# Performance work log

Measured on AMD Instinct MI355X. Metric: run time of the kernel, lower is better.

Reference implementation:

```python
import jax, jax.numpy as jnp
import numpy as np

N, C, K = 400000, 32, 27
EPS = 1e-5


def sparse_conv(feats, W, nbr, mask):
    # feats [N,Cin], W [K,Cin,Cout], nbr [N,K] int, mask [N,K] bool
    g = feats[nbr] * mask[..., None]          # gather: [N,K,Cin]
    return jnp.einsum('nki,kio->no', g, W)    # per-offset GEMM + scatter-accumulate


def batchnorm(x, gamma, beta):
    # MinkowskiBatchNorm over all active points (axis 0), training-mode stats
    mean = jnp.mean(x, axis=0)
    var = jnp.var(x, axis=0)
    return (x - mean) * jax.lax.rsqrt(var + EPS) * gamma + beta


def setup_inputs() -> dict:
    key = jax.random.key(0)
    ks = jax.random.split(key, 8)
    feats = jax.random.normal(ks[0], (N, C), dtype=jnp.float32)
    nbr = jax.random.randint(ks[1], (N, K), 0, N, dtype=jnp.int32)
    mask = jax.random.randint(ks[2], (N, K), 0, 2, dtype=jnp.int32).astype(bool)
    scale = 1.0 / np.sqrt(K * C)
    W1 = jax.random.normal(ks[3], (K, C, C), dtype=jnp.float32) * scale
    W2 = jax.random.normal(ks[4], (K, C, C), dtype=jnp.float32) * scale
    gamma1 = jnp.ones((C,), jnp.float32)
    beta1 = jnp.zeros((C,), jnp.float32)
    gamma2 = jnp.ones((C,), jnp.float32)
    beta2 = jnp.zeros((C,), jnp.float32)
    return {"feats": feats, "W1": W1, "gamma1": gamma1, "beta1": beta1,
            "W2": W2, "gamma2": gamma2, "beta2": beta2,
            "nbr": nbr, "mask": mask}


def reference(feats, W1, gamma1, beta1, W2, gamma2, beta2, nbr, mask):
    h = sparse_conv(feats, W1, nbr, mask)
    h = jax.nn.relu(batchnorm(h, gamma1, beta1))
    h = sparse_conv(h, W2, nbr, mask)
    h = batchnorm(h, gamma2, beta2)
    # in_ch == out_ch -> identity residual (no downsample branch)
    return jax.nn.relu(h + feats)
```

## Files before the change

### kernel.cpp

```cpp
#include <hip/hip_runtime.h>

#define NPTS 400000
#define KOFF 27

typedef __attribute__((ext_vector_type(8))) __bf16 bf16x8;
typedef __attribute__((ext_vector_type(16))) float v16f;

__device__ __forceinline__ float bf2f(unsigned short u) {
  union { unsigned int i; float f; } v; v.i = ((unsigned int)u) << 16; return v.f;
}
__device__ __forceinline__ unsigned short f2bf(float f) {
  union { float f; unsigned int i; } v; v.f = f;
  unsigned int x = v.i;
  return (unsigned short)((x + 0x7FFFu + ((x >> 16) & 1u)) >> 16);
}

__global__ void prep_feats(const float* __restrict__ feats, unsigned short* __restrict__ Xb,
                           unsigned short* __restrict__ H1, float* __restrict__ statszero) {
  int idx = blockIdx.x * 256 + threadIdx.x;
  const float4* f4 = (const float4*)feats;
  float4 a = f4[2 * idx], b = f4[2 * idx + 1];
  union { unsigned short u[8]; uint4 v; } p;
  p.u[0] = f2bf(a.x); p.u[1] = f2bf(a.y); p.u[2] = f2bf(a.z); p.u[3] = f2bf(a.w);
  p.u[4] = f2bf(b.x); p.u[5] = f2bf(b.y); p.u[6] = f2bf(b.z); p.u[7] = f2bf(b.w);
  ((uint4*)Xb)[idx] = p.v;
  if (blockIdx.x == 0) {
    if (threadIdx.x < 32) {
      Xb[(size_t)NPTS * 32 + threadIdx.x] = 0;
      H1[(size_t)NPTS * 32 + threadIdx.x] = 0;
    }
    if (threadIdx.x < 128) statszero[threadIdx.x] = 0.f;
  }
}

__global__ void prep_nbr(const int* __restrict__ nbr, const int* __restrict__ mask,
                         int* __restrict__ nbrT) {
  int n = blockIdx.x * 256 + threadIdx.x;
  if (n >= NPTS) return;
  #pragma unroll
  for (int k = 0; k < KOFF; ++k) {
    int j = nbr[(size_t)n * KOFF + k];
    int m = mask[(size_t)n * KOFF + k];
    nbrT[(size_t)k * NPTS + n] = (m != 0) ? j : NPTS;
  }
}

__global__ void prep_w(const float* __restrict__ W1, const float* __restrict__ W2,
                       unsigned short* __restrict__ WT1, unsigned short* __restrict__ WT2) {
  int i = blockIdx.x * 256 + threadIdx.x;
  if (i >= 27 * 1024) return;
  int k = i >> 10, r = i & 1023, o = r >> 5, ic = r & 31;
  int src = k * 1024 + ic * 32 + o;
  WT1[i] = f2bf(W1[src]);
  WT2[i] = f2bf(W2[src]);
}

__global__ __launch_bounds__(256, 4) void conv_mfma(
    const unsigned short* __restrict__ X,
    const int* __restrict__ nbrT,
    const unsigned short* __restrict__ WT,
    unsigned short* __restrict__ Hout,
    float* __restrict__ stats)
{
  const int lane = threadIdx.x & 63;
  const int wv   = threadIdx.x >> 6;
  const int col  = lane & 31;
  const int hf   = lane >> 5;
  const int n0   = (blockIdx.x * 4 + wv) * 32;

  v16f acc;
  #pragma unroll
  for (int i = 0; i < 16; ++i) acc[i] = 0.0f;

  const int* nb = nbrT + n0 + col;
  const bf16x8* wp = (const bf16x8*)(WT + col * 32 + hf * 8);

  #pragma unroll 4
  for (int k = 0; k < KOFF; ++k) {
    int row = nb[k * NPTS];
    const bf16x8* ap = (const bf16x8*)(X + (size_t)row * 32 + hf * 8);
    bf16x8 a0 = ap[0];
    bf16x8 a1 = ap[2];
    bf16x8 b0 = wp[k * 128];
    bf16x8 b1 = wp[k * 128 + 2];
    acc = __builtin_amdgcn_mfma_f32_32x32x16_bf16(a0, b0, acc, 0, 0, 0);
    acc = __builtin_amdgcn_mfma_f32_32x32x16_bf16(a1, b1, acc, 0, 0, 0);
  }

  float s = 0.f, q = 0.f;
  #pragma unroll
  for (int r = 0; r < 16; ++r) {
    float v = acc[r];
    s += v; q += v * v;
    int rw = (r & 3) + 8 * (r >> 2) + 4 * hf;
    Hout[(size_t)(n0 + rw) * 32 + col] = f2bf(v);
  }
  s += __shfl_xor(s, 32);
  q += __shfl_xor(q, 32);
  __shared__ float redS[4][32];
  __shared__ float redQ[4][32];
  if (lane < 32) { redS[wv][col] = s; redQ[wv][col] = q; }
  __syncthreads();
  if (threadIdx.x < 64) {
    int t = threadIdx.x & 31;
    float v = (threadIdx.x < 32)
      ? (redS[0][t] + redS[1][t] + redS[2][t] + redS[3][t])
      : (redQ[0][t] + redQ[1][t] + redQ[2][t] + redQ[3][t]);
    atomicAdd(&stats[threadIdx.x], v);
  }
}

__global__ void finalize_bn(const float* __restrict__ stats, const float* __restrict__ gamma,
                            const float* __restrict__ beta, float* __restrict__ sb) {
  int t = threadIdx.x;
  if (t < 32) {
    float mean = stats[t] * (1.f / NPTS);
    float var  = stats[t + 32] * (1.f / NPTS) - mean * mean;
    float rstd = rsqrtf(var + 1e-5f);
    float sc = gamma[t] * rstd;
    sb[t] = sc;
    sb[t + 32] = beta[t] - mean * sc;
  }
}

__global__ void bn_relu_inplace(unsigned short* __restrict__ H, const float* __restrict__ sb) {
  int idx = blockIdx.x * 256 + threadIdx.x;
  uint4 v = ((uint4*)H)[idx];
  union { uint4 v; unsigned short u[8]; } p; p.v = v;
  int baseo = (idx * 8) & 31;
  #pragma unroll
  for (int j = 0; j < 8; ++j) {
    float f = bf2f(p.u[j]);
    f = fmaxf(f * sb[baseo + j] + sb[32 + baseo + j], 0.f);
    p.u[j] = f2bf(f);
  }
  ((uint4*)H)[idx] = p.v;
}

__global__ void bn_res_relu_out(const unsigned short* __restrict__ H2, const float* __restrict__ feats,
                                const float* __restrict__ sb, float* __restrict__ out) {
  int idx = blockIdx.x * 256 + threadIdx.x;
  uint4 v = ((const uint4*)H2)[idx];
  union { uint4 v; unsigned short u[8]; } p; p.v = v;
  int baseo = (idx * 8) & 31;
  const float4* f4 = (const float4*)feats;
  float4 fa = f4[2 * idx], fb = f4[2 * idx + 1];
  float4 o0, o1;
  float* fav = (float*)&fa; float* fbv = (float*)&fb;
  float* o0v = (float*)&o0; float* o1v = (float*)&o1;
  #pragma unroll
  for (int j = 0; j < 4; ++j)
    o0v[j] = fmaxf(bf2f(p.u[j]) * sb[baseo + j] + sb[32 + baseo + j] + fav[j], 0.f);
  #pragma unroll
  for (int j = 0; j < 4; ++j)
    o1v[j] = fmaxf(bf2f(p.u[4 + j]) * sb[baseo + 4 + j] + sb[32 + baseo + 4 + j] + fbv[j], 0.f);
  ((float4*)out)[2 * idx] = o0;
  ((float4*)out)[2 * idx + 1] = o1;
}

extern "C" void kernel_launch(void* const* d_in, const int* in_sizes, int n_in,
                              void* d_out, int out_size, void* d_ws, size_t ws_size,
                              hipStream_t stream) {
  const float* feats  = (const float*)d_in[0];
  const float* W1     = (const float*)d_in[1];
  const float* gamma1 = (const float*)d_in[2];
  const float* beta1  = (const float*)d_in[3];
  const float* W2     = (const float*)d_in[4];
  const float* gamma2 = (const float*)d_in[5];
  const float* beta2  = (const float*)d_in[6];
  const int*   nbr    = (const int*)d_in[7];
  const int*   mask   = (const int*)d_in[8];

  char* ws = (char*)d_ws;
  const size_t XB = ((size_t)(NPTS + 1) * 32 * 2 + 255) & ~(size_t)255;
  unsigned short* Xb   = (unsigned short*)(ws);
  unsigned short* H1   = (unsigned short*)(ws + XB);
  int*            nbrT = (int*)(ws + 2 * XB);
  size_t off = 2 * XB + (size_t)KOFF * NPTS * 4;
  unsigned short* WT1 = (unsigned short*)(ws + off); off += 27 * 1024 * 2;
  unsigned short* WT2 = (unsigned short*)(ws + off); off += 27 * 1024 * 2;
  float* stats1 = (float*)(ws + off); off += 256;
  float* stats2 = (float*)(ws + off); off += 256;
  float* sb1    = (float*)(ws + off); off += 256;
  float* sb2    = (float*)(ws + off); off += 256;
  unsigned short* H2 = Xb;

  prep_feats<<<6250, 256, 0, stream>>>(feats, Xb, H1, stats1);
  prep_nbr<<<1563, 256, 0, stream>>>(nbr, mask, nbrT);
  prep_w<<<108, 256, 0, stream>>>(W1, W2, WT1, WT2);

  conv_mfma<<<3125, 256, 0, stream>>>(Xb, nbrT, WT1, H1, stats1);
  finalize_bn<<<1, 64, 0, stream>>>(stats1, gamma1, beta1, sb1);
  bn_relu_inplace<<<6250, 256, 0, stream>>>(H1, sb1);

  conv_mfma<<<3125, 256, 0, stream>>>(H1, nbrT, WT2, H2, stats2);
  finalize_bn<<<1, 64, 0, stream>>>(stats2, gamma2, beta2, sb2);
  bn_res_relu_out<<<6250, 256, 0, stream>>>(H2, feats, sb2, (float*)d_out);
}
```

Baseline: 448.7 us.

## Switch conv to 16x16x32 MFMA with LDS-staged weights and fuse BN finalize

The conv kernel moves from 32x32x16 MFMA tiles to 16x16x32 tiles in 1024-thread blocks. All 27 offset weight fragments are preloaded into LDS in a lane-ready layout, and the next neighbor index is prefetched on each iteration. The neighbor-table transpose now goes through shared memory so global reads and writes are coalesced. The separate finalize_bn launches are folded into the BN/ReLU kernels, which each recompute scale and shift per block. This cuts global weight loads and launch count, at the cost of a 54KB LDS load per block and a heavy register and occupancy demand from the 1024-thread blocks.

```diff
diff --git a/kernel.cpp b/kernel.cpp
--- a/kernel.cpp
+++ b/kernel.cpp
@@ -4,7 +4,7 @@
 #define KOFF 27
 
 typedef __attribute__((ext_vector_type(8))) __bf16 bf16x8;
-typedef __attribute__((ext_vector_type(16))) float v16f;
+typedef __attribute__((ext_vector_type(4))) float v4f;
 
 __device__ __forceinline__ float bf2f(unsigned short u) {
   union { unsigned int i; float f; } v; v.i = ((unsigned int)u) << 16; return v.f;
@@ -35,95 +35,122 @@
 
 __global__ void prep_nbr(const int* __restrict__ nbr, const int* __restrict__ mask,
                          int* __restrict__ nbrT) {
-  int n = blockIdx.x * 256 + threadIdx.x;
-  if (n >= NPTS) return;
-  #pragma unroll
-  for (int k = 0; k < KOFF; ++k) {
-    int j = nbr[(size_t)n * KOFF + k];
-    int m = mask[(size_t)n * KOFF + k];
-    nbrT[(size_t)k * NPTS + n] = (m != 0) ? j : NPTS;
+  __shared__ int tile[256 * KOFF];
+  int p0 = blockIdx.x * 256;
+  int cnt = (NPTS - p0 < 256) ? (NPTS - p0) : 256;
+  int total = cnt * KOFF;
+  for (int i = threadIdx.x; i < total; i += 256) {
+    int j = nbr[(size_t)p0 * KOFF + i];
+    int mk = mask[(size_t)p0 * KOFF + i];
+    tile[i] = (mk != 0) ? j : NPTS;
+  }
+  __syncthreads();
+  int t = threadIdx.x;
+  if (t < cnt) {
+    #pragma unroll
+    for (int k = 0; k < KOFF; ++k)
+      nbrT[(size_t)k * NPTS + p0 + t] = tile[t * KOFF + k];
   }
 }
 
 __global__ void prep_w(const float* __restrict__ W1, const float* __restrict__ W2,
-                       unsigned short* __restrict__ WT1, unsigned short* __restrict__ WT2) {
-  int i = blockIdx.x * 256 + threadIdx.x;
-  if (i >= 27 * 1024) return;
-  int k = i >> 10, r = i & 1023, o = r >> 5, ic = r & 31;
-  int src = k * 1024 + ic * 32 + o;
-  WT1[i] = f2bf(W1[src]);
-  WT2[i] = f2bf(W2[src]);
-}
-
-__global__ __launch_bounds__(256, 4) void conv_mfma(
+                       unsigned short* __restrict__ WL1, unsigned short* __restrict__ WL2) {
+  int idx = blockIdx.x * 256 + threadIdx.x;
+  if (idx >= KOFF * 1024) return;
+  int k = idx >> 10, r = idx & 1023;
+  int h = r >> 9, rr = r & 511;
+  int lane = rr >> 3, j = rr & 7;
+  int i_ch = (lane >> 4) * 8 + j;
+  int o_ch = h * 16 + (lane & 15);
+  int src = k * 1024 + i_ch * 32 + o_ch;
+  WL1[idx] = f2bf(W1[src]);
+  WL2[idx] = f2bf(W2[src]);
+}
+
+__global__ __launch_bounds__(1024, 8) void conv_mfma16(
     const unsigned short* __restrict__ X,
     const int* __restrict__ nbrT,
-    const unsigned short* __restrict__ WT,
+    const unsigned short* __restrict__ WL,
     unsigned short* __restrict__ Hout,
     float* __restrict__ stats)
 {
-  const int lane = threadIdx.x & 63;
-  const int wv   = threadIdx.x >> 6;
-  const int col  = lane & 31;
-  const int hf   = lane >> 5;
-  const int n0   = (blockIdx.x * 4 + wv) * 32;
-
-  v16f acc;
-  #pragma unroll
-  for (int i = 0; i < 16; ++i) acc[i] = 0.0f;
-
-  const int* nb = nbrT + n0 + col;
-  const bf16x8* wp = (const bf16x8*)(WT + col * 32 + hf * 8);
-
-  #pragma unroll 4
-  for (int k = 0; k < KOFF; ++k) {
-    int row = nb[k * NPTS];
-    const bf16x8* ap = (const bf16x8*)(X + (size_t)row * 32 + hf * 8);
-    bf16x8 a0 = ap[0];
-    bf16x8 a1 = ap[2];
-    bf16x8 b0 = wp[k * 128];
-    bf16x8 b1 = wp[k * 128 + 2];
-    acc = __builtin_amdgcn_mfma_f32_32x32x16_bf16(a0, b0, acc, 0, 0, 0);
-    acc = __builtin_amdgcn_mfma_f32_32x32x16_bf16(a1, b1, acc, 0, 0, 0);
-  }
-
-  float s = 0.f, q = 0.f;
-  #pragma unroll
-  for (int r = 0; r < 16; ++r) {
-    float v = acc[r];
-    s += v; q += v * v;
-    int rw = (r & 3) + 8 * (r >> 2) + 4 * hf;
-    Hout[(size_t)(n0 + rw) * 32 + col] = f2bf(v);
-  }
-  s += __shfl_xor(s, 32);
-  q += __shfl_xor(q, 32);
-  __shared__ float redS[4][32];
-  __shared__ float redQ[4][32];
-  if (lane < 32) { redS[wv][col] = s; redQ[wv][col] = q; }
-  __syncthreads();
-  if (threadIdx.x < 64) {
-    int t = threadIdx.x & 31;
-    float v = (threadIdx.x < 32)
-      ? (redS[0][t] + redS[1][t] + redS[2][t] + redS[3][t])
-      : (redQ[0][t] + redQ[1][t] + redQ[2][t] + redQ[3][t]);
-    atomicAdd(&stats[threadIdx.x], v);
-  }
-}
-
-__global__ void finalize_bn(const float* __restrict__ stats, const float* __restrict__ gamma,
-                            const float* __restrict__ beta, float* __restrict__ sb) {
-  int t = threadIdx.x;
-  if (t < 32) {
+  __shared__ unsigned char wlds[KOFF * 2048];
+  __shared__ float redS[16][32];
+  __shared__ float redQ[16][32];
+
+  const int tid = threadIdx.x;
+  {
+    const uint4* src = (const uint4*)WL;
+    uint4* dst = (uint4*)wlds;
+    for (int i = tid; i < KOFF * 128; i += 1024) dst[i] = src[i];
+  }
+  __syncthreads();
+
+  const int lane = tid & 63;
+  const int wv   = tid >> 6;
+  const int m    = lane & 15;
+  const int q    = lane >> 4;
+  const int n0   = blockIdx.x * 256 + wv * 16;
+  const bool active = (n0 < NPTS);
+
+  v4f acc0 = {0.f, 0.f, 0.f, 0.f};
+  v4f acc1 = {0.f, 0.f, 0.f, 0.f};
+  float s0 = 0.f, s1 = 0.f, qq0 = 0.f, qq1 = 0.f;
+
+  if (active) {
+    const int* nbp = nbrT + n0 + m;
+    const unsigned short* xq = X + q * 8;
+    const bf16x8* wfrag = (const bf16x8*)wlds;
+    int nb = nbp[0];
+    #pragma unroll 3
+    for (int k = 0; k < KOFF; ++k) {
+      int nb_next = (k < KOFF - 1) ? nbp[(k + 1) * NPTS] : 0;
+      bf16x8 a  = *(const bf16x8*)(xq + (size_t)nb * 32);
+      bf16x8 b0 = wfrag[(k * 2 + 0) * 64 + lane];
+      bf16x8 b1 = wfrag[(k * 2 + 1) * 64 + lane];
+      acc0 = __builtin_amdgcn_mfma_f32_16x16x32_bf16(a, b0, acc0, 0, 0, 0);
+      acc1 = __builtin_amdgcn_mfma_f32_16x16x32_bf16(a, b1, acc1, 0, 0, 0);
+      nb = nb_next;
+    }
+    #pragma unroll
+    for (int r = 0; r < 4; ++r) {
+      float v0 = acc0[r], v1 = acc1[r];
+      s0 += v0; s1 += v1; qq0 += v0 * v0; qq1 += v1 * v1;
+      size_t pt = (size_t)(n0 + q * 4 + r);
+      Hout[pt * 32 + m]      = f2bf(v0);
+      Hout[pt * 32 + 16 + m] = f2bf(v1);
+    }
+  }
+  s0  += __shfl_xor(s0, 16);  s0  += __shfl_xor(s0, 32);
+  s1  += __shfl_xor(s1, 16);  s1  += __shfl_xor(s1, 32);
+  qq0 += __shfl_xor(qq0, 16); qq0 += __shfl_xor(qq0, 32);
+  qq1 += __shfl_xor(qq1, 16); qq1 += __shfl_xor(qq1, 32);
+  if (lane < 16) {
+    redS[wv][m] = s0; redS[wv][m + 16] = s1;
+    redQ[wv][m] = qq0; redQ[wv][m + 16] = qq1;
+  }
+  __syncthreads();
+  if (tid < 64) {
+    int t = tid & 31;
+    float a = 0.f;
+    if (tid < 32) { for (int w = 0; w < 16; ++w) a += redS[w][t]; }
+    else          { for (int w = 0; w < 16; ++w) a += redQ[w][t]; }
+    atomicAdd(&stats[tid], a);
+  }
+}
+
+__global__ void bn_relu_fused(unsigned short* __restrict__ H, const float* __restrict__ stats,
+                              const float* __restrict__ gamma, const float* __restrict__ beta) {
+  __shared__ float sb[64];
+  if (threadIdx.x < 32) {
+    int t = threadIdx.x;
     float mean = stats[t] * (1.f / NPTS);
     float var  = stats[t + 32] * (1.f / NPTS) - mean * mean;
     float rstd = rsqrtf(var + 1e-5f);
     float sc = gamma[t] * rstd;
-    sb[t] = sc;
-    sb[t + 32] = beta[t] - mean * sc;
-  }
-}
-
-__global__ void bn_relu_inplace(unsigned short* __restrict__ H, const float* __restrict__ sb) {
+    sb[t] = sc; sb[t + 32] = beta[t] - mean * sc;
+  }
+  __syncthreads();
   int idx = blockIdx.x * 256 + threadIdx.x;
   uint4 v = ((uint4*)H)[idx];
   union { uint4 v; unsigned short u[8]; } p; p.v = v;
@@ -138,7 +165,18 @@
 }
 
 __global__ void bn_res_relu_out(const unsigned short* __restrict__ H2, const float* __restrict__ feats,
-                                const float* __restrict__ sb, float* __restrict__ out) {
+                                const float* __restrict__ stats, const float* __restrict__ gamma,
+                                const float* __restrict__ beta, float* __restrict__ out) {
+  __shared__ float sb[64];
+  if (threadIdx.x < 32) {
+    int t = threadIdx.x;
+    float mean = stats[t] * (1.f / NPTS);
+    float var  = stats[t + 32] * (1.f / NPTS) - mean * mean;
+    float rstd = rsqrtf(var + 1e-5f);
+    float sc = gamma[t] * rstd;
+    sb[t] = sc; sb[t + 32] = beta[t] - mean * sc;
+  }
+  __syncthreads();
   int idx = blockIdx.x * 256 + threadIdx.x;
   uint4 v = ((const uint4*)H2)[idx];
   union { uint4 v; unsigned short u[8]; } p; p.v = v;
@@ -177,23 +215,19 @@
   unsigned short* H1   = (unsigned short*)(ws + XB);
   int*            nbrT = (int*)(ws + 2 * XB);
   size_t off = 2 * XB + (size_t)KOFF * NPTS * 4;
-  unsigned short* WT1 = (unsigned short*)(ws + off); off += 27 * 1024 * 2;
-  unsigned short* WT2 = (unsigned short*)(ws + off); off += 27 * 1024 * 2;
+  unsigned short* WL1 = (unsigned short*)(ws + off); off += KOFF * 1024 * 2;
+  unsigned short* WL2 = (unsigned short*)(ws + off); off += KOFF * 1024 * 2;
   float* stats1 = (float*)(ws + off); off += 256;
   float* stats2 = (float*)(ws + off); off += 256;
-  float* sb1    = (float*)(ws + off); off += 256;
-  float* sb2    = (float*)(ws + off); off += 256;
   unsigned short* H2 = Xb;
 
   prep_feats<<<6250, 256, 0, stream>>>(feats, Xb, H1, stats1);
   prep_nbr<<<1563, 256, 0, stream>>>(nbr, mask, nbrT);
-  prep_w<<<108, 256, 0, stream>>>(W1, W2, WT1, WT2);
-
-  conv_mfma<<<3125, 256, 0, stream>>>(Xb, nbrT, WT1, H1, stats1);
-  finalize_bn<<<1, 64, 0, stream>>>(stats1, gamma1, beta1, sb1);
-  bn_relu_inplace<<<6250, 256, 0, stream>>>(H1, sb1);
-
-  conv_mfma<<<3125, 256, 0, stream>>>(H1, nbrT, WT2, H2, stats2);
-  finalize_bn<<<1, 64, 0, stream>>>(stats2, gamma2, beta2, sb2);
-  bn_res_relu_out<<<6250, 256, 0, stream>>>(H2, feats, sb2, (float*)d_out);
-}
+  prep_w<<<108, 256, 0, stream>>>(W1, W2, WL1, WL2);
+
+  conv_mfma16<<<1563, 1024, 0, stream>>>(Xb, nbrT, WL1, H1, stats1);
+  bn_relu_fused<<<6250, 256, 0, stream>>>(H1, stats1, gamma1, beta1);
+
+  conv_mfma16<<<1563, 1024, 0, stream>>>(H1, nbrT, WL2, H2, stats2);
+  bn_res_relu_out<<<6250, 256, 0, stream>>>(H2, feats, stats2, gamma2, beta2, (float*)d_out);
+}
```

After: 455.6 us. About the same (+1.5%).
